# Performance work log

Hardware: AMD Instinct MI355X
Metric: run time of the kernel (lower is better)

## Reference

```python
import jax
import jax.numpy as jnp
import numpy as np
from jax.scipy.special import logsumexp

B, T, D, K = 2048, 512, 32, 10  # K = n_labels + 1
LN_EPS = 1e-5


def setup_inputs() -> dict:
    key = jax.random.key(0)
    ks = jax.random.split(key, 8)
    x = jax.random.normal(ks[0], (B, T, D), dtype=jnp.float32)
    labels = jax.random.randint(ks[1], (B, T), 0, K)
    attention_mask = jnp.ones((B, T), dtype=jnp.int32)
    # Linear(32, K) params
    W = (jax.random.normal(ks[2], (K, D), dtype=jnp.float32) * 0.05)
    b = jnp.zeros((K,), dtype=jnp.float32)
    # LayerNorm(K) params
    gamma = jnp.ones((K,), dtype=jnp.float32)
    beta = jnp.zeros((K,), dtype=jnp.float32)
    # torchcrf params: init uniform(-0.1, 0.1)
    start_transitions = jax.random.uniform(ks[3], (K,), minval=-0.1, maxval=0.1)
    end_transitions = jax.random.uniform(ks[4], (K,), minval=-0.1, maxval=0.1)
    transitions = jax.random.uniform(ks[5], (K, K), minval=-0.1, maxval=0.1)
    return {
        "x": x, "labels": labels, "attention_mask": attention_mask,
        "W": W, "b": b, "gamma": gamma, "beta": beta,
        "start_transitions": start_transitions,
        "end_transitions": end_transitions,
        "transitions": transitions,
    }


def _emissions(x, W, b, gamma, beta):
    h = jnp.einsum("btd,kd->btk", x, W) + b
    mu = jnp.mean(h, axis=-1, keepdims=True)
    var = jnp.mean((h - mu) ** 2, axis=-1, keepdims=True)
    return (h - mu) * jax.lax.rsqrt(var + LN_EPS) * gamma + beta


def _crf_llh(em, tags, mask, start_t, end_t, trans):
    # em: [B,T,K], tags: [B,T] int, mask: [B,T] int (mask[:,0]==1)
    Bn = em.shape[0]
    maskf = mask.astype(em.dtype)
    bidx = jnp.arange(Bn)
    # numerator: score of the gold path
    first = tags[:, 0]
    num = start_t[first] + em[bidx, 0, first]
    trans_sc = trans[tags[:, :-1], tags[:, 1:]]                          # [B,T-1]
    em_sc = jnp.take_along_axis(em, tags[:, :, None], axis=2)[:, :, 0]   # [B,T]
    num = num + jnp.sum((trans_sc + em_sc[:, 1:]) * maskf[:, 1:], axis=1)
    last_idx = jnp.sum(mask, axis=1).astype(jnp.int32) - 1
    last_tag = tags[bidx, last_idx]
    num = num + end_t[last_tag]
    # denominator: forward algorithm (logsumexp recurrence over time)
    score0 = start_t + em[:, 0]                                          # [B,K]

    def step(score, inp):
        em_t, m_t = inp
        nxt = logsumexp(score[:, :, None] + trans[None] + em_t[:, None, :], axis=1)
        score = jnp.where(m_t[:, None] > 0, nxt, score)
        return score, None

    score, _ = jax.lax.scan(step, score0,
                            (jnp.swapaxes(em, 0, 1)[1:], mask.T[1:]))
    log_z = logsumexp(score + end_t, axis=1)
    return num - log_z


def _viterbi(em, start_t, end_t, trans):
    # torchcrf.decode with no mask -> full-length decode
    Bn = em.shape[0]
    score0 = start_t + em[:, 0]                                          # [B,K]

    def vstep(score, em_t):
        broad = score[:, :, None] + trans                                # [B,K,K]
        idx = jnp.argmax(broad, axis=1)                                  # [B,K]
        score = jnp.max(broad, axis=1) + em_t
        return score, idx

    score, history = jax.lax.scan(vstep, score0, jnp.swapaxes(em, 0, 1)[1:])
    score = score + end_t
    last = jnp.argmax(score, axis=1)                                     # [B]

    def back(tag, hist_t):
        prev = jnp.take_along_axis(hist_t, tag[:, None], axis=1)[:, 0]
        return prev, prev

    _, prevs = jax.lax.scan(back, last, history, reverse=True)           # [T-1,B]
    path = jnp.concatenate([prevs, last[None]], axis=0).T                # [B,T]
    return path.astype(jnp.int64)


def reference(x, labels, attention_mask, W, b, gamma, beta,
              start_transitions, end_transitions, transitions):
    em = _emissions(x, W, b, gamma, beta)
    llh = _crf_llh(em, labels, attention_mask,
                   start_transitions, end_transitions, transitions)
    loss = -jnp.sum(llh)  # torchcrf default reduction='sum'; loss = -llh
    path = _viterbi(em, start_transitions, end_transitions, transitions)
    return loss, path
```

## Files before the change

kernel.cpp:

```cpp
#include <hip/hip_runtime.h>
#include <hip/hip_bf16.h>

#define B_ 2048
#define T_ 512
#define D_ 32
#define K_ 10
#define LN_EPS 1e-5f
#define CH_ 64
#define NCH_ (T_ / CH_)


#define SWZPAT(i) (((i) << 5) | 0x10)

__device__ __forceinline__ void viterbi_cands(float v, const float Tc[K_],
                                              float c[K_], float& best)
{
    c[0] = __int_as_float(__builtin_amdgcn_ds_swizzle(__float_as_int(v), SWZPAT(0))) + Tc[0];
    c[1] = __int_as_float(__builtin_amdgcn_ds_swizzle(__float_as_int(v), SWZPAT(1))) + Tc[1];
    c[2] = __int_as_float(__builtin_amdgcn_ds_swizzle(__float_as_int(v), SWZPAT(2))) + Tc[2];
    c[3] = __int_as_float(__builtin_amdgcn_ds_swizzle(__float_as_int(v), SWZPAT(3))) + Tc[3];
    c[4] = __int_as_float(__builtin_amdgcn_ds_swizzle(__float_as_int(v), SWZPAT(4))) + Tc[4];
    c[5] = __int_as_float(__builtin_amdgcn_ds_swizzle(__float_as_int(v), SWZPAT(5))) + Tc[5];
    c[6] = __int_as_float(__builtin_amdgcn_ds_swizzle(__float_as_int(v), SWZPAT(6))) + Tc[6];
    c[7] = __int_as_float(__builtin_amdgcn_ds_swizzle(__float_as_int(v), SWZPAT(7))) + Tc[7];
    c[8] = __int_as_float(__builtin_amdgcn_ds_swizzle(__float_as_int(v), SWZPAT(8))) + Tc[8];
    c[9] = __int_as_float(__builtin_amdgcn_ds_swizzle(__float_as_int(v), SWZPAT(9))) + Tc[9];
    float m0 = fmaxf(c[0], fmaxf(c[1], c[2]));
    float m1 = fmaxf(c[3], fmaxf(c[4], c[5]));
    float m2 = fmaxf(c[6], fmaxf(c[7], c[8]));
    best = fmaxf(fmaxf(m0, m1), fmaxf(m2, c[9]));
}

__device__ __forceinline__ int argmax_first(const float c[K_], float best)
{
    int bi = 9;
    bi = (c[8] == best) ? 8 : bi;
    bi = (c[7] == best) ? 7 : bi;
    bi = (c[6] == best) ? 6 : bi;
    bi = (c[5] == best) ? 5 : bi;
    bi = (c[4] == best) ? 4 : bi;
    bi = (c[3] == best) ? 3 : bi;
    bi = (c[2] == best) ? 2 : bi;
    bi = (c[1] == best) ? 1 : bi;
    bi = (c[0] == best) ? 0 : bi;
    return bi;
}

__global__ __launch_bounds__(256) void emis_kernel(
    const float* __restrict__ x, const float* __restrict__ W,
    const float* __restrict__ bb, const float* __restrict__ gamma,
    const float* __restrict__ beta, float* __restrict__ em)
{
    __shared__ float sW[K_ * D_ + 3 * K_];
    for (int i = threadIdx.x; i < K_ * D_ + 3 * K_; i += blockDim.x) {
        float v;
        if (i < K_ * D_)             v = W[i];
        else if (i < K_ * D_ + K_)   v = bb[i - K_ * D_];
        else if (i < K_ * D_ + 2*K_) v = gamma[i - K_ * D_ - K_];
        else                         v = beta[i - K_ * D_ - 2 * K_];
        sW[i] = v;
    }
    __syncthreads();
    int row = blockIdx.x * blockDim.x + threadIdx.x;
    const float4* xr = reinterpret_cast<const float4*>(x + (size_t)row * D_);
    float4 xv[8];
    #pragma unroll
    for (int i = 0; i < 8; i++) xv[i] = xr[i];
    float h[K_];
    #pragma unroll
    for (int k = 0; k < K_; k++) {
        float acc = 0.f;
        #pragma unroll
        for (int i = 0; i < 8; i++) {
            acc = fmaf(xv[i].x, sW[k * D_ + 4 * i + 0], acc);
            acc = fmaf(xv[i].y, sW[k * D_ + 4 * i + 1], acc);
            acc = fmaf(xv[i].z, sW[k * D_ + 4 * i + 2], acc);
            acc = fmaf(xv[i].w, sW[k * D_ + 4 * i + 3], acc);
        }
        h[k] = acc + sW[K_ * D_ + k];
    }
    float mu = 0.f;
    #pragma unroll
    for (int k = 0; k < K_; k++) mu += h[k];
    mu = mu / (float)K_;
    float var = 0.f;
    #pragma unroll
    for (int k = 0; k < K_; k++) { float d = h[k] - mu; var += d * d; }
    var = var / (float)K_;
    float r = 1.0f / sqrtf(var + LN_EPS);
    float e[K_];
    #pragma unroll
    for (int k = 0; k < K_; k++)
        e[k] = (h[k] - mu) * r * sW[K_ * D_ + K_ + k] + sW[K_ * D_ + 2 * K_ + k];
    float2* eo = reinterpret_cast<float2*>(em + (size_t)row * K_);
    #pragma unroll
    for (int k = 0; k < 5; k++) eo[k] = make_float2(e[2 * k], e[2 * k + 1]);
}

__global__ __launch_bounds__(64) void vscan_kernel(
    const float* __restrict__ em, const float* __restrict__ startt,
    const float* __restrict__ trans, float* __restrict__ bnd)
{
    __shared__ __align__(16) float emL[2 * 4 * 644];
    __shared__ float str[110];

    const int lane = threadIdx.x;
    const int g  = lane >> 4;
    const int gl = lane & 15;
    const int b  = blockIdx.x * 4 + g;
    const int jj = (gl < K_) ? gl : (K_ - 1);

    for (int i = lane; i < 110; i += 64)
        str[i] = (i < 100) ? trans[i] : startt[i - 100];

    const int il = gl;
    const float* gsrc = em + (size_t)b * T_ * K_;
    float* emLg0 = emL + g * 644;
    float* emLg1 = emL + (4 + g) * 644;
    float4 rg[10];
    {
        const float4* p = reinterpret_cast<const float4*>(gsrc);
        #pragma unroll
        for (int it = 0; it < 10; ++it) rg[it] = p[il + 16 * it];
        float4* d4 = reinterpret_cast<float4*>(emLg0);
        #pragma unroll
        for (int it = 0; it < 10; ++it) d4[il + 16 * it] = rg[it];
    }
    {
        const float4* p = reinterpret_cast<const float4*>(gsrc + 640);
        #pragma unroll
        for (int it = 0; it < 10; ++it) rg[it] = p[il + 16 * it];
    }
    __builtin_amdgcn_wave_barrier();

    float Tc[K_];
    #pragma unroll
    for (int i = 0; i < K_; i++) Tc[i] = str[i * K_ + jj];

    float v = str[100 + jj] + emLg0[jj];
    bnd[((size_t)0 * 512 + blockIdx.x) * 64 + lane] = v;
    float em_nx = emLg0[K_ + jj];

    int t = 1;
    #pragma unroll 1
    for (int c = 0; c < NCH_; ++c) {
        float* emLg  = (c & 1) ? emLg1 : emLg0;
        float* emLgN = (c & 1) ? emLg0 : emLg1;
        int tcStart = (c == 0) ? 1 : 0;
        #pragma unroll 1
        for (int tc = tcStart; tc < CH_; ++tc) {
            float em_t = em_nx;
            if (tc + 1 < CH_) em_nx = emLg[(tc + 1) * K_ + jj];
            float cc[K_], best;
            viterbi_cands(v, Tc, cc, best);
            v = best + em_t;
            if ((t & 31) == 0)
                bnd[((size_t)(t >> 5) * 512 + blockIdx.x) * 64 + lane] = v;
            ++t;
        }
        if (c + 1 < NCH_) {
            float4* d4 = reinterpret_cast<float4*>(emLgN);
            #pragma unroll
            for (int it = 0; it < 10; ++it) d4[il + 16 * it] = rg[it];
            if (c + 2 < NCH_) {
                const float4* p = reinterpret_cast<const float4*>(gsrc + (size_t)(c + 2) * 640);
                #pragma unroll
                for (int it = 0; it < 10; ++it) rg[it] = p[il + 16 * it];
            }
            __builtin_amdgcn_wave_barrier();
            em_nx = emLgN[jj];
        }
    }
}

__global__ __launch_bounds__(64) void vseg_kernel(
    const float* __restrict__ em, const int* __restrict__ labels,
    const float* __restrict__ startt, const float* __restrict__ endt,
    const float* __restrict__ trans, const float* __restrict__ bnd,
    unsigned char* __restrict__ hist, float* __restrict__ numpart,
    int* __restrict__ last_out)
{
    __shared__ __align__(16) float emB[4 * 336];
    __shared__ int   labB[4][33];
    __shared__ float str[120];

    const int lane = threadIdx.x;
    const int g  = lane >> 4;
    const int gl = lane & 15;
    const int s   = blockIdx.x >> 9;
    const int blk = blockIdx.x & 511;
    const int b0  = blk * 4;
    const int b   = b0 + g;
    const int jj  = (gl < K_) ? gl : (K_ - 1);
    const int t_lo   = s * 32 + 1;
    const int nsteps = (s == 15) ? 31 : 32;

    for (int i = lane; i < 120; i += 64) {
        float vv;
        if (i < 100)      vv = trans[i];
        else if (i < 110) vv = startt[i - 100];
        else              vv = endt[i - 110];
        str[i] = vv;
    }
    for (int i = lane; i < 640; i += 64) {
        int gg = i / 160;
        int ff = i - gg * 160;
        float2 w = *reinterpret_cast<const float2*>(
            em + ((size_t)(b0 + gg) * T_ + t_lo) * K_ + (size_t)ff * 2);
        *reinterpret_cast<float2*>(&emB[gg * 336 + ff * 2]) = w;
    }
    for (int i = lane; i < 132; i += 64) {
        int gg = i / 33;
        int k  = i - gg * 33;
        if (k <= nsteps)
            labB[gg][k] = labels[(size_t)(b0 + gg) * T_ + t_lo - 1 + k];
    }
    __builtin_amdgcn_wave_barrier();
    __syncthreads();

    float Tc[K_];
    #pragma unroll
    for (int i = 0; i < K_; i++) Tc[i] = str[i * K_ + jj];

    float v = bnd[((size_t)s * 512 + blk) * 64 + lane];
    float em_nx = emB[g * 336 + jj];
    float num = 0.f;
    int prev = labB[g][0];

    unsigned char* hb = hist + (size_t)b * 16 + gl;

    #pragma unroll 1
    for (int step = 0; step < nsteps; ++step) {
        int t = t_lo + step;
        float em_t = em_nx;
        if (step + 1 < nsteps) em_nx = emB[g * 336 + (step + 1) * K_ + jj];

        float cc[K_], best;
        viterbi_cands(v, Tc, cc, best);
        int bi = argmax_first(cc, best);
        v = best + em_t;

        hb[(size_t)t * (B_ * 16)] = (unsigned char)bi;
        if (gl == 10) {
            int lab_t = labB[g][step + 1];
            num += str[prev * K_ + lab_t] + emB[g * 336 + step * K_ + lab_t];
            prev = lab_t;
        }
    }
    if (gl == 10) numpart[(size_t)s * B_ + b] = num;

    if (s == 15) {
        float cc[K_];
        #pragma unroll
        for (int i = 0; i < K_; i++) cc[i] = __int_as_float(
            __builtin_amdgcn_ds_swizzle(__float_as_int(v), SWZPAT(0))) ;
        float d0 = __int_as_float(__builtin_amdgcn_ds_swizzle(__float_as_int(v), SWZPAT(0))) + str[110+0];
        float d1 = __int_as_float(__builtin_amdgcn_ds_swizzle(__float_as_int(v), SWZPAT(1))) + str[110+1];
        float d2 = __int_as_float(__builtin_amdgcn_ds_swizzle(__float_as_int(v), SWZPAT(2))) + str[110+2];
        float d3 = __int_as_float(__builtin_amdgcn_ds_swizzle(__float_as_int(v), SWZPAT(3))) + str[110+3];
        float d4 = __int_as_float(__builtin_amdgcn_ds_swizzle(__float_as_int(v), SWZPAT(4))) + str[110+4];
        float d5 = __int_as_float(__builtin_amdgcn_ds_swizzle(__float_as_int(v), SWZPAT(5))) + str[110+5];
        float d6 = __int_as_float(__builtin_amdgcn_ds_swizzle(__float_as_int(v), SWZPAT(6))) + str[110+6];
        float d7 = __int_as_float(__builtin_amdgcn_ds_swizzle(__float_as_int(v), SWZPAT(7))) + str[110+7];
        float d8 = __int_as_float(__builtin_amdgcn_ds_swizzle(__float_as_int(v), SWZPAT(8))) + str[110+8];
        float d9 = __int_as_float(__builtin_amdgcn_ds_swizzle(__float_as_int(v), SWZPAT(9))) + str[110+9];
        float m0 = fmaxf(d0, fmaxf(d1, d2));
        float m1 = fmaxf(d3, fmaxf(d4, d5));
        float m2 = fmaxf(d6, fmaxf(d7, d8));
        float best = fmaxf(fmaxf(m0, m1), fmaxf(m2, d9));
        int bi = 9;
        bi = (d8 == best) ? 8 : bi;
        bi = (d7 == best) ? 7 : bi;
        bi = (d6 == best) ? 6 : bi;
        bi = (d5 == best) ? 5 : bi;
        bi = (d4 == best) ? 4 : bi;
        bi = (d3 == best) ? 3 : bi;
        bi = (d2 == best) ? 2 : bi;
        bi = (d1 == best) ? 1 : bi;
        bi = (d0 == best) ? 0 : bi;
        if (gl == 0) last_out[b] = bi;
    }
}

__global__ __launch_bounds__(640) void aprob_kernel(
    const float* __restrict__ em, const float* __restrict__ trans,
    float* __restrict__ P_pr, float* __restrict__ P_ps)
{
    __shared__ float tile[320 * 65];
    const int tid = threadIdx.x;
    const int seg = blockIdx.x >> 5;
    const int b0  = (blockIdx.x & 31) * 64;
    const int t_lo = seg * 32 + 1;
    const int nt   = (seg == 15) ? 31 : 32;

    #pragma unroll
    for (int q = 0; q < 8; ++q) {
        int f   = q * 640 + tid;
        int bi  = f / 80;
        int f4i = f - bi * 80;
        float4 vv = *reinterpret_cast<const float4*>(
            em + ((size_t)(b0 + bi) * T_ + t_lo) * K_ + (size_t)f4i * 4);
        int fi = f4i * 4;
        tile[(fi + 0) * 65 + bi] = vv.x;
        tile[(fi + 1) * 65 + bi] = vv.y;
        tile[(fi + 2) * 65 + bi] = vv.z;
        tile[(fi + 3) * 65 + bi] = vv.w;
    }
    __syncthreads();

    const int w     = tid >> 6;
    const int lanel = tid & 63;
    const int seq   = b0 + lanel;

    float Ee[K_][K_];
    #pragma unroll
    for (int i = 0; i < K_; i++)
        #pragma unroll
        for (int j = 0; j < K_; j++)
            Ee[i][j] = __expf(trans[i * K_ + j]);

    float r[K_];
    #pragma unroll
    for (int j = 0; j < K_; j++) r[j] = (j == w) ? 1.f : 0.f;
    float scale = 0.f;

    #pragma unroll 1
    for (int off = 0; off < nt; ++off) {
        float ec[K_];
        #pragma unroll
        for (int k = 0; k < K_; k++) ec[k] = tile[(off * K_ + k) * 65 + lanel];
        float mx = fmaxf(fmaxf(fmaxf(ec[0], ec[1]), fmaxf(ec[2], ec[3])),
                  fmaxf(fmaxf(fmaxf(ec[4], ec[5]), fmaxf(ec[6], ec[7])), fmaxf(ec[8], ec[9])));
        float eem[K_];
        #pragma unroll
        for (int j = 0; j < K_; j++) eem[j] = __expf(ec[j] - mx);
        float acc[K_];
        #pragma unroll
        for (int j = 0; j < K_; j++) acc[j] = r[0] * Ee[0][j];
        #pragma unroll
        for (int i = 1; i < K_; i++)
            #pragma unroll
            for (int j = 0; j < K_; j++) acc[j] = fmaf(r[i], Ee[i][j], acc[j]);
        #pragma unroll
        for (int j = 0; j < K_; j++) r[j] = acc[j] * eem[j];
        scale += mx;
        if ((off & 7) == 7) {
            float rm = fmaxf(fmaxf(fmaxf(r[0], r[1]), fmaxf(r[2], r[3])),
                      fmaxf(fmaxf(fmaxf(r[4], r[5]), fmaxf(r[6], r[7])), fmaxf(r[8], r[9])));
            float inv = 1.0f / rm;
            #pragma unroll
            for (int j = 0; j < K_; j++) r[j] *= inv;
            scale += __logf(rm);
        }
    }
    float rm = fmaxf(fmaxf(fmaxf(r[0], r[1]), fmaxf(r[2], r[3])),
              fmaxf(fmaxf(fmaxf(r[4], r[5]), fmaxf(r[6], r[7])), fmaxf(r[8], r[9])));
    float inv = 1.0f / rm;
    scale += __logf(rm);
    #pragma unroll
    for (int j = 0; j < K_; j++)
        P_pr[(((size_t)seg * K_ + w) * K_ + j) * B_ + seq] = r[j] * inv;
    P_ps[((size_t)seg * K_ + w) * B_ + seq] = scale;
}

__global__ __launch_bounds__(64) void bfold_kernel(
    const float* __restrict__ em, const int* __restrict__ labels,
    const float* __restrict__ startt, const float* __restrict__ endt,
    const float* __restrict__ numpart, const float* __restrict__ P_pr,
    const float* __restrict__ P_ps, float* __restrict__ llh)
{
    int seq = blockIdx.x * 64 + threadIdx.x;
    float f[K_];
    float v0[K_];
    #pragma unroll
    for (int j = 0; j < K_; j++) v0[j] = startt[j] + em[(size_t)seq * (T_ * K_) + j];
    float m = fmaxf(fmaxf(fmaxf(v0[0], v0[1]), fmaxf(v0[2], v0[3])),
             fmaxf(fmaxf(fmaxf(v0[4], v0[5]), fmaxf(v0[6], v0[7])), fmaxf(v0[8], v0[9])));
    #pragma unroll
    for (int j = 0; j < K_; j++) f[j] = __expf(v0[j] - m);
    float fs = m;

    #pragma unroll 1
    for (int s = 0; s < 16; ++s) {
        float ps[K_];
        #pragma unroll
        for (int i = 0; i < K_; i++) ps[i] = P_ps[((size_t)s * K_ + i) * B_ + seq];
        float pm = fmaxf(fmaxf(fmaxf(ps[0], ps[1]), fmaxf(ps[2], ps[3])),
                  fmaxf(fmaxf(fmaxf(ps[4], ps[5]), fmaxf(ps[6], ps[7])), fmaxf(ps[8], ps[9])));
        float gc[K_];
        #pragma unroll
        for (int i = 0; i < K_; i++) gc[i] = f[i] * __expf(ps[i] - pm);
        float nf[K_];
        #pragma unroll
        for (int j = 0; j < K_; j++) nf[j] = 0.f;
        #pragma unroll
        for (int i = 0; i < K_; i++)
            #pragma unroll
            for (int j = 0; j < K_; j++)
                nf[j] = fmaf(gc[i], P_pr[(((size_t)s * K_ + i) * K_ + j) * B_ + seq], nf[j]);
        float nm = fmaxf(fmaxf(fmaxf(nf[0], nf[1]), fmaxf(nf[2], nf[3])),
                  fmaxf(fmaxf(fmaxf(nf[4], nf[5]), fmaxf(nf[6], nf[7])), fmaxf(nf[8], nf[9])));
        float inv = 1.0f / nm;
        #pragma unroll
        for (int j = 0; j < K_; j++) f[j] = nf[j] * inv;
        fs += pm + __logf(nm);
    }
    float z = 0.f;
    #pragma unroll
    for (int j = 0; j < K_; j++) z = fmaf(f[j], __expf(endt[j]), z);
    float logz = __logf(z) + fs;

    int l0   = labels[(size_t)seq * T_];
    int l511 = labels[(size_t)seq * T_ + T_ - 1];
    float num = startt[l0] + em[(size_t)seq * (T_ * K_) + l0] + endt[l511];
    #pragma unroll
    for (int s = 0; s < 16; ++s) num += numpart[(size_t)s * B_ + seq];

    llh[seq] = num - logz;
}

__global__ __launch_bounds__(256) void compose_kernel(
    const unsigned char* __restrict__ hist, unsigned long long* __restrict__ Fmaps)
{
    int tid = blockIdx.x * 256 + threadIdx.x;
    int seg = tid >> 11;
    int b   = tid & 2047;
    int t_hi = (seg == 15) ? 511 : (seg * 32 + 32);
    int t_lo = seg * 32 + 1;
    const int4* h4 = reinterpret_cast<const int4*>(hist);
    unsigned long long F = 0x9876543210ull;
    #pragma unroll 4
    for (int t = t_hi; t >= t_lo; --t) {
        int4 mv = h4[(size_t)t * B_ + b];
        unsigned long long Fn = 0;
        #pragma unroll
        for (int j = 0; j < 10; ++j) {
            int idx = (int)((F >> (4 * j)) & 15ull);
            unsigned word = (idx >= 8) ? (unsigned)mv.z : ((idx >= 4) ? (unsigned)mv.y : (unsigned)mv.x);
            unsigned long long nib = (word >> ((idx & 3) * 8)) & 15u;
            Fn |= nib << (4 * j);
        }
        F = Fn;
    }
    Fmaps[(size_t)seg * B_ + b] = F;
}

__global__ __launch_bounds__(256) void foldb_kernel(
    const unsigned long long* __restrict__ Fmaps, const int* __restrict__ last,
    unsigned long long* __restrict__ bndpk)
{
    int b = blockIdx.x * 256 + threadIdx.x;
    int tag = last[b];
    unsigned long long pk = 0;
    #pragma unroll
    for (int s = 15; s >= 0; --s) {
        unsigned long long F = Fmaps[(size_t)s * B_ + b];
        tag = (int)((F >> (4 * tag)) & 15ull);
        pk |= ((unsigned long long)tag) << (4 * s);
    }
    bndpk[b] = pk;
}

__global__ __launch_bounds__(64) void expand_kernel(
    const unsigned char* __restrict__ hist, const int* __restrict__ last,
    const unsigned long long* __restrict__ bndpk, float* __restrict__ path)
{
    __shared__ float tile[64][33];
    const int seg  = blockIdx.x >> 5;
    const int bc   = blockIdx.x & 31;
    const int lane = threadIdx.x;
    const int b = bc * 64 + lane;
    const int t_hi = (seg == 15) ? 511 : (seg * 32 + 32);
    const int t_lo = seg * 32 + 1;
    int tag = (seg == 15) ? last[b] : (int)((bndpk[b] >> (4 * (seg + 1))) & 15ull);
    if (seg == 15) tile[lane][31] = (float)tag;
    const int4* h4 = reinterpret_cast<const int4*>(hist);
    #pragma unroll 4
    for (int t = t_hi; t >= t_lo; --t) {
        int4 mv = h4[(size_t)t * B_ + b];
        unsigned word = (tag >= 8) ? (unsigned)mv.z : ((tag >= 4) ? (unsigned)mv.y : (unsigned)mv.x);
        tag = (int)((word >> ((tag & 3) * 8)) & 15u);
        tile[lane][t - 1 - seg * 32] = (float)tag;
    }
    __syncthreads();
    float* pb = path + ((size_t)(bc * 64)) * T_ + seg * 32;
    #pragma unroll 4
    for (int rr = 0; rr < 32; ++rr) {
        int r = rr * 2 + (lane >> 5);
        int c = lane & 31;
        pb[(size_t)r * T_ + c] = tile[r][c];
    }
}

__global__ __launch_bounds__(256) void loss_kernel(
    const float* __restrict__ llh, float* __restrict__ out)
{
    __shared__ float red[256];
    float s = 0.f;
    for (int i = threadIdx.x; i < B_; i += 256) s += llh[i];
    red[threadIdx.x] = s;
    __syncthreads();
    for (int off = 128; off > 0; off >>= 1) {
        if (threadIdx.x < off) red[threadIdx.x] += red[threadIdx.x + off];
        __syncthreads();
    }
    if (threadIdx.x == 0) out[0] = -red[0];
}

extern "C" void kernel_launch(void* const* d_in, const int* in_sizes, int n_in,
                              void* d_out, int out_size, void* d_ws, size_t ws_size,
                              hipStream_t stream)
{
    const float* x      = (const float*)d_in[0];
    const int*   labels = (const int*)d_in[1];
    const float* W      = (const float*)d_in[3];
    const float* bb     = (const float*)d_in[4];
    const float* gamma  = (const float*)d_in[5];
    const float* beta   = (const float*)d_in[6];
    const float* startt = (const float*)d_in[7];
    const float* endt   = (const float*)d_in[8];
    const float* trans  = (const float*)d_in[9];
    float* out = (float*)d_out;

    char* ws = (char*)d_ws;
    float*              em      = (float*)(ws);
    unsigned char*      hist    = (unsigned char*)(ws + 41943040);
    float*              P_pr    = (float*)(ws + 58720256);
    float*              P_ps    = (float*)(ws + 71827456);
    float*              llh     = (float*)(ws + 73138176);
    int*                last    = (int*)(ws + 73146368);
    unsigned long long* Fmaps   = (unsigned long long*)(ws + 73154560);
    unsigned long long* bndpk   = (unsigned long long*)(ws + 73416704);
    float*              numpart = (float*)(ws + 73433088);
    float*              bnd     = (float*)(ws + 58720256);

    emis_kernel<<<(B_ * T_) / 256, 256, 0, stream>>>(x, W, bb, gamma, beta, em);
    vscan_kernel<<<B_ / 4, 64, 0, stream>>>(em, startt, trans, bnd);
    vseg_kernel<<<16 * (B_ / 4), 64, 0, stream>>>(em, labels, startt, endt, trans,
                                                  bnd, hist, numpart, last);
    aprob_kernel<<<16 * 32, 640, 0, stream>>>(em, trans, P_pr, P_ps);
    bfold_kernel<<<B_ / 64, 64, 0, stream>>>(em, labels, startt, endt, numpart,
                                             P_pr, P_ps, llh);
    compose_kernel<<<16 * B_ / 256, 256, 0, stream>>>(hist, Fmaps);
    foldb_kernel<<<B_ / 256, 256, 0, stream>>>(Fmaps, last, bndpk);
    expand_kernel<<<16 * 32, 64, 0, stream>>>(hist, last, bndpk, out + 1);
    loss_kernel<<<1, 256, 0, stream>>>(llh, out);
}
```

Measured before the change: 286.0 us.

## Run Viterbi boundary scan with one sequence per thread and register prefetch

The vscan kernel changes from 16 lanes per sequence (ds_swizzle broadcasts, LDS double buffering) to one thread per sequence. Each thread holds the full 10x10 transition matrix and the 10-state score vector in registers and prefetches emission rows four steps ahead from global memory. The boundary array layout becomes [segment][state][batch], and vseg is updated to read it. The launch shrinks to 32 blocks of 64 threads, so parallelism is much lower but there is no cross-lane traffic. bfold's segment loop is also unrolled by 2, and a dead swizzle loop is removed.

```diff
diff --git a/kernel.cpp b/kernel.cpp
--- a/kernel.cpp
+++ b/kernel.cpp
@@ -6,8 +6,6 @@
 #define D_ 32
 #define K_ 10
 #define LN_EPS 1e-5f
-#define CH_ 64
-#define NCH_ (T_ / CH_)
 
 
 #define SWZPAT(i) (((i) << 5) | 0x10)
@@ -97,79 +95,75 @@
     for (int k = 0; k < 5; k++) eo[k] = make_float2(e[2 * k], e[2 * k + 1]);
 }
 
+struct VScan {
+    float v[K_];
+    float T[K_][K_];
+    const float* eb;
+    float* bnd;
+    int b;
+
+    __device__ __forceinline__ void loadrow(float (&e)[K_], int t) {
+        const float* rp = eb + (size_t)t * K_;
+        #pragma unroll
+        for (int q = 0; q < 5; ++q) {
+            float2 w = *reinterpret_cast<const float2*>(rp + 2 * q);
+            e[2 * q] = w.x; e[2 * q + 1] = w.y;
+        }
+    }
+    __device__ __forceinline__ void step(float (&e)[K_], int t) {
+        float nv[K_];
+        #pragma unroll
+        for (int j = 0; j < K_; j++) {
+            float m = v[0] + T[0][j];
+            #pragma unroll
+            for (int i = 1; i < K_; i++) m = fmaxf(m, v[i] + T[i][j]);
+            nv[j] = m + e[j];
+        }
+        #pragma unroll
+        for (int j = 0; j < K_; j++) v[j] = nv[j];
+        if ((t & 31) == 0 && t <= 480) {
+            #pragma unroll
+            for (int k = 0; k < K_; k++)
+                bnd[((size_t)(t >> 5) * K_ + k) * B_ + b] = v[k];
+        }
+        int tr = t + 4; if (tr > 511) tr = 511;
+        loadrow(e, tr);
+    }
+};
+
 __global__ __launch_bounds__(64) void vscan_kernel(
     const float* __restrict__ em, const float* __restrict__ startt,
     const float* __restrict__ trans, float* __restrict__ bnd)
 {
-    __shared__ __align__(16) float emL[2 * 4 * 644];
-    __shared__ float str[110];
-
-    const int lane = threadIdx.x;
-    const int g  = lane >> 4;
-    const int gl = lane & 15;
-    const int b  = blockIdx.x * 4 + g;
-    const int jj = (gl < K_) ? gl : (K_ - 1);
-
-    for (int i = lane; i < 110; i += 64)
-        str[i] = (i < 100) ? trans[i] : startt[i - 100];
-
-    const int il = gl;
-    const float* gsrc = em + (size_t)b * T_ * K_;
-    float* emLg0 = emL + g * 644;
-    float* emLg1 = emL + (4 + g) * 644;
-    float4 rg[10];
+    VScan S;
+    S.b   = blockIdx.x * 64 + threadIdx.x;
+    S.eb  = em + (size_t)S.b * (T_ * K_);
+    S.bnd = bnd;
+    #pragma unroll
+    for (int i = 0; i < K_; i++)
+        #pragma unroll
+        for (int j = 0; j < K_; j++)
+            S.T[i][j] = trans[i * K_ + j];
+
     {
-        const float4* p = reinterpret_cast<const float4*>(gsrc);
-        #pragma unroll
-        for (int it = 0; it < 10; ++it) rg[it] = p[il + 16 * it];
-        float4* d4 = reinterpret_cast<float4*>(emLg0);
-        #pragma unroll
-        for (int it = 0; it < 10; ++it) d4[il + 16 * it] = rg[it];
-    }
-    {
-        const float4* p = reinterpret_cast<const float4*>(gsrc + 640);
-        #pragma unroll
-        for (int it = 0; it < 10; ++it) rg[it] = p[il + 16 * it];
-    }
-    __builtin_amdgcn_wave_barrier();
-
-    float Tc[K_];
-    #pragma unroll
-    for (int i = 0; i < K_; i++) Tc[i] = str[i * K_ + jj];
-
-    float v = str[100 + jj] + emLg0[jj];
-    bnd[((size_t)0 * 512 + blockIdx.x) * 64 + lane] = v;
-    float em_nx = emLg0[K_ + jj];
-
-    int t = 1;
+        float e0[K_];
+        S.loadrow(e0, 0);
+        #pragma unroll
+        for (int j = 0; j < K_; j++) S.v[j] = startt[j] + e0[j];
+        #pragma unroll
+        for (int k = 0; k < K_; k++)
+            bnd[((size_t)0 * K_ + k) * B_ + S.b] = S.v[k];
+    }
+    float eA[K_], eB[K_], eC[K_], eD[K_];
+    S.loadrow(eA, 1); S.loadrow(eB, 2); S.loadrow(eC, 3); S.loadrow(eD, 4);
+
     #pragma unroll 1
-    for (int c = 0; c < NCH_; ++c) {
-        float* emLg  = (c & 1) ? emLg1 : emLg0;
-        float* emLgN = (c & 1) ? emLg0 : emLg1;
-        int tcStart = (c == 0) ? 1 : 0;
-        #pragma unroll 1
-        for (int tc = tcStart; tc < CH_; ++tc) {
-            float em_t = em_nx;
-            if (tc + 1 < CH_) em_nx = emLg[(tc + 1) * K_ + jj];
-            float cc[K_], best;
-            viterbi_cands(v, Tc, cc, best);
-            v = best + em_t;
-            if ((t & 31) == 0)
-                bnd[((size_t)(t >> 5) * 512 + blockIdx.x) * 64 + lane] = v;
-            ++t;
-        }
-        if (c + 1 < NCH_) {
-            float4* d4 = reinterpret_cast<float4*>(emLgN);
-            #pragma unroll
-            for (int it = 0; it < 10; ++it) d4[il + 16 * it] = rg[it];
-            if (c + 2 < NCH_) {
-                const float4* p = reinterpret_cast<const float4*>(gsrc + (size_t)(c + 2) * 640);
-                #pragma unroll
-                for (int it = 0; it < 10; ++it) rg[it] = p[il + 16 * it];
-            }
-            __builtin_amdgcn_wave_barrier();
-            em_nx = emLgN[jj];
-        }
+    for (int c = 0; c < 128; ++c) {
+        int t0 = 4 * c + 1;
+        S.step(eA, t0);
+        S.step(eB, t0 + 1);
+        S.step(eC, t0 + 2);
+        S.step(eD, t0 + 3);
     }
 }
 
@@ -222,7 +216,7 @@
     #pragma unroll
     for (int i = 0; i < K_; i++) Tc[i] = str[i * K_ + jj];
 
-    float v = bnd[((size_t)s * 512 + blk) * 64 + lane];
+    float v = bnd[((size_t)s * K_ + jj) * B_ + b];
     float em_nx = emB[g * 336 + jj];
     float num = 0.f;
     int prev = labB[g][0];
@@ -250,10 +244,6 @@
     if (gl == 10) numpart[(size_t)s * B_ + b] = num;
 
     if (s == 15) {
-        float cc[K_];
-        #pragma unroll
-        for (int i = 0; i < K_; i++) cc[i] = __int_as_float(
-            __builtin_amdgcn_ds_swizzle(__float_as_int(v), SWZPAT(0))) ;
         float d0 = __int_as_float(__builtin_amdgcn_ds_swizzle(__float_as_int(v), SWZPAT(0))) + str[110+0];
         float d1 = __int_as_float(__builtin_amdgcn_ds_swizzle(__float_as_int(v), SWZPAT(1))) + str[110+1];
         float d2 = __int_as_float(__builtin_amdgcn_ds_swizzle(__float_as_int(v), SWZPAT(2))) + str[110+2];
@@ -380,7 +370,7 @@
     for (int j = 0; j < K_; j++) f[j] = __expf(v0[j] - m);
     float fs = m;
 
-    #pragma unroll 1
+    #pragma unroll 2
     for (int s = 0; s < 16; ++s) {
         float ps[K_];
         #pragma unroll
@@ -535,7 +525,7 @@
     float*              bnd     = (float*)(ws + 58720256);
 
     emis_kernel<<<(B_ * T_) / 256, 256, 0, stream>>>(x, W, bb, gamma, beta, em);
-    vscan_kernel<<<B_ / 4, 64, 0, stream>>>(em, startt, trans, bnd);
+    vscan_kernel<<<B_ / 64, 64, 0, stream>>>(em, startt, trans, bnd);
     vseg_kernel<<<16 * (B_ / 4), 64, 0, stream>>>(em, labels, startt, endt, trans,
                                                   bnd, hist, numpart, last);
     aprob_kernel<<<16 * 32, 640, 0, stream>>>(em, trans, P_pr, P_ps);
```

Result: slower. 467.1 us (+63.3%).
